# Optimization experiments

Measured on AMD Instinct MI355X. Metric: run time of the kernel, lower is better.

Reference implementation:

```python
import jax, jax.numpy as jnp
import numpy as np

D = 512  # feature_dim


def setup_inputs() -> dict:
    key = jax.random.key(0)
    ks = jax.random.split(key, 10)
    s = 1.0 / np.sqrt(D)
    s2 = 1.0 / np.sqrt(2 * D)
    return {
        "X": jax.random.normal(ks[0], (8, 2048, D), dtype=jnp.float32),
        "Y": jax.random.normal(ks[1], (8, 2048, D), dtype=jnp.float32),
        "W_xq": jax.random.uniform(ks[2], (D, D), jnp.float32, -s, s),
        "b_xq": jax.random.uniform(ks[3], (D,), jnp.float32, -s, s),
        "W_yq": jax.random.uniform(ks[4], (D, D), jnp.float32, -s, s),
        "b_yq": jax.random.uniform(ks[5], (D,), jnp.float32, -s, s),
        "W_fk": jax.random.uniform(ks[6], (D, 2 * D), jnp.float32, -s2, s2),
        "b_fk": jax.random.uniform(ks[7], (D,), jnp.float32, -s2, s2),
        "W_fv": jax.random.uniform(ks[8], (D, 2 * D), jnp.float32, -s2, s2),
        "b_fv": jax.random.uniform(ks[9], (D,), jnp.float32, -s2, s2),
    }


def reference(X, Y, W_xq, b_xq, W_yq, b_yq, W_fk, b_fk, W_fv, b_fv):
    # Dropout is evaluated in eval mode (identity).
    scale = 1.0 / jnp.sqrt(jnp.asarray(D, X.dtype))
    Q1 = jnp.einsum('bsd,ed->bse', X, W_xq) + b_xq  # [B,S,D]
    Q2 = jnp.einsum('bsd,ed->bse', Y, W_yq) + b_yq
    Q_cat = jnp.concatenate([Q1, Q2], axis=-1)      # [B,S,2D]
    K_f = jnp.einsum('bsc,ec->bse', Q_cat, W_fk) + b_fk
    V_f = jnp.einsum('bsc,ec->bse', Q_cat, W_fv) + b_fv

    def attend(Q):
        scores = jnp.einsum('bqd,bkd->bqk', Q, K_f) * scale  # [B,S,S]
        A = jax.nn.softmax(scores, axis=-1)
        return jnp.einsum('bqk,bkd->bqd', A, V_f)

    U_A1 = X + attend(Q1)
    U_A2 = Y + attend(Q2)
    return U_A1 + U_A2
```

## Files before the change

### kernel.cpp

```cpp
#include <hip/hip_runtime.h>


#define B_    8
#define S_    2048
#define D_    512
#define M_TOT (B_ * S_)

typedef __bf16 bf16_t;
typedef __bf16 bf16x8 __attribute__((ext_vector_type(8)));
typedef __bf16 bf16x4 __attribute__((ext_vector_type(4)));
typedef float  f32x4  __attribute__((ext_vector_type(4)));

typedef __attribute__((address_space(1))) const void* gas_cv;
typedef __attribute__((address_space(3))) void*       las_v;

__device__ __forceinline__ f32x4 mfma16(bf16x8 a, bf16x8 b, f32x4 c) {
    return __builtin_amdgcn_mfma_f32_16x16x32_bf16(a, b, c, 0, 0, 0);
}
__device__ __forceinline__ void load_lds16(const void* g, void* l) {
    __builtin_amdgcn_global_load_lds((gas_cv)g, (las_v)l, 16, 0, 0);
}

__global__ __launch_bounds__(256) void k_cvt(
    const float* __restrict__ X, const float* __restrict__ Y,
    const float* __restrict__ Wxq, const float* __restrict__ Wyq,
    const float* __restrict__ Wfk, const float* __restrict__ Wfv,
    bf16_t* __restrict__ Xb, bf16_t* __restrict__ Yb,
    bf16_t* __restrict__ Wb)
{
    const int tid = blockIdx.x * 256 + threadIdx.x;
    const int n4 = M_TOT * 512 / 4;
    for (int i = tid; i < n4; i += 2048 * 256) {
        const float4 x = *(const float4*)(X + (size_t)i * 4);
        bf16x4 px = { (bf16_t)x.x, (bf16_t)x.y, (bf16_t)x.z, (bf16_t)x.w };
        *(bf16x4*)(Xb + (size_t)i * 4) = px;
        const float4 y = *(const float4*)(Y + (size_t)i * 4);
        bf16x4 py = { (bf16_t)y.x, (bf16_t)y.y, (bf16_t)y.z, (bf16_t)y.w };
        *(bf16x4*)(Yb + (size_t)i * 4) = py;
    }
    if (tid < 393216) {
        const float* src; int sj;
        if (tid < 65536)       { src = Wxq; sj = tid; }
        else if (tid < 131072) { src = Wyq; sj = tid - 65536; }
        else if (tid < 262144) { src = Wfk; sj = tid - 131072; }
        else                   { src = Wfv; sj = tid - 262144; }
        const float4 v = *(const float4*)(src + (size_t)sj * 4);
        bf16x4 p = { (bf16_t)v.x, (bf16_t)v.y, (bf16_t)v.z, (bf16_t)v.w };
        *(bf16x4*)(Wb + (size_t)tid * 4) = p;
    }
}

__global__ __launch_bounds__(256) void k_qgemm_bb(
    const bf16_t* __restrict__ Xb, const bf16_t* __restrict__ Yb,
    const bf16_t* __restrict__ Wb,
    const float* __restrict__ bxq, const float* __restrict__ byq,
    bf16_t* __restrict__ Qcat)
{
    __shared__ __attribute__((aligned(16))) bf16_t Al[128 * 32];
    __shared__ __attribute__((aligned(16))) bf16_t Bl[128 * 32];
    const int m0 = blockIdx.y * 128;
    const int n0 = blockIdx.x * 128;
    const bool second = (n0 >= 512);
    const bf16_t* A   = second ? Yb : Xb;
    const bf16_t* W   = Wb + (second ? 262144 : 0);
    const float* bias = second ? byq : bxq;
    const int nw = n0 & 511;
    const int t    = threadIdx.x;
    const int lane = t & 63;
    const int wv   = t >> 6;
    const int wm   = (wv & 1) * 64;
    const int wn   = (wv >> 1) * 64;
    const int l15  = lane & 15;
    const int quad = lane >> 4;

    const int ar0 = t >> 2,          ac0 = (t & 3) * 8;
    const int ar1 = (256 + t) >> 2,  ac1 = ((256 + t) & 3) * 8;

    f32x4 acc[4][4] = {};

    for (int k0 = 0; k0 < 512; k0 += 32) {
        __syncthreads();
        load_lds16(A + (size_t)(m0 + ar0) * 512 + k0 + ac0, Al + t * 8);
        load_lds16(A + (size_t)(m0 + ar1) * 512 + k0 + ac1, Al + (256 + t) * 8);
        load_lds16(W + (size_t)(nw + ar0) * 512 + k0 + ac0, Bl + t * 8);
        load_lds16(W + (size_t)(nw + ar1) * 512 + k0 + ac1, Bl + (256 + t) * 8);
        __syncthreads();
        bf16x8 af[4], bfr[4];
#pragma unroll
        for (int i = 0; i < 4; ++i)
            af[i] = *(const bf16x8*)(Al + (wm + i * 16 + l15) * 32 + quad * 8);
#pragma unroll
        for (int i = 0; i < 4; ++i)
            bfr[i] = *(const bf16x8*)(Bl + (wn + i * 16 + l15) * 32 + quad * 8);
#pragma unroll
        for (int mt = 0; mt < 4; ++mt)
#pragma unroll
            for (int nt = 0; nt < 4; ++nt)
                acc[mt][nt] = mfma16(af[mt], bfr[nt], acc[mt][nt]);
    }

#pragma unroll
    for (int nt = 0; nt < 4; ++nt) {
        const int col  = n0 + wn + nt * 16 + l15;
        const float bv = bias[col & 511];
#pragma unroll
        for (int mt = 0; mt < 4; ++mt) {
            const int rowb = m0 + wm + mt * 16 + quad * 4;
#pragma unroll
            for (int r = 0; r < 4; ++r)
                Qcat[(size_t)(rowb + r) * 1024 + col] = (bf16_t)(acc[mt][nt][r] + bv);
        }
    }
}

__global__ __launch_bounds__(256) void k_kvgemm_bb(
    const bf16_t* __restrict__ Qcat,
    const bf16_t* __restrict__ Wfkb, const float* __restrict__ bfk,
    const bf16_t* __restrict__ Wfvb, const float* __restrict__ bfv,
    bf16_t* __restrict__ Kf, bf16_t* __restrict__ Vt)
{
    __shared__ __attribute__((aligned(16))) union {
        struct { bf16_t Al[128 * 32]; bf16_t Bl[128 * 32]; } g;
        bf16_t T[128 * 132];
    } sm;
    const int m0 = blockIdx.y * 128;
    const int n0 = blockIdx.x * 128;
    const bool isV = (n0 >= 512);
    const bf16_t* W   = isV ? Wfvb : Wfkb;
    const float* bias = isV ? bfv : bfk;
    const int nw = n0 & 511;
    const int t    = threadIdx.x;
    const int lane = t & 63;
    const int wv   = t >> 6;
    const int wm   = (wv & 1) * 64;
    const int wn   = (wv >> 1) * 64;
    const int l15  = lane & 15;
    const int quad = lane >> 4;

    const int ar0 = t >> 2,          ac0 = (t & 3) * 8;
    const int ar1 = (256 + t) >> 2,  ac1 = ((256 + t) & 3) * 8;

    f32x4 acc[4][4] = {};

    for (int k0 = 0; k0 < 1024; k0 += 32) {
        __syncthreads();
        load_lds16(Qcat + (size_t)(m0 + ar0) * 1024 + k0 + ac0, sm.g.Al + t * 8);
        load_lds16(Qcat + (size_t)(m0 + ar1) * 1024 + k0 + ac1, sm.g.Al + (256 + t) * 8);
        load_lds16(W + (size_t)(nw + ar0) * 1024 + k0 + ac0, sm.g.Bl + t * 8);
        load_lds16(W + (size_t)(nw + ar1) * 1024 + k0 + ac1, sm.g.Bl + (256 + t) * 8);
        __syncthreads();
        bf16x8 af[4], bfr[4];
#pragma unroll
        for (int i = 0; i < 4; ++i)
            af[i] = *(const bf16x8*)(sm.g.Al + (wm + i * 16 + l15) * 32 + quad * 8);
#pragma unroll
        for (int i = 0; i < 4; ++i)
            bfr[i] = *(const bf16x8*)(sm.g.Bl + (wn + i * 16 + l15) * 32 + quad * 8);
#pragma unroll
        for (int mt = 0; mt < 4; ++mt)
#pragma unroll
            for (int nt = 0; nt < 4; ++nt)
                acc[mt][nt] = mfma16(af[mt], bfr[nt], acc[mt][nt]);
    }

    if (!isV) {
#pragma unroll
        for (int nt = 0; nt < 4; ++nt) {
            const int col  = n0 + wn + nt * 16 + l15;
            const float bv = bias[col];
#pragma unroll
            for (int mt = 0; mt < 4; ++mt) {
                const int rowb = m0 + wm + mt * 16 + quad * 4;
#pragma unroll
                for (int r = 0; r < 4; ++r)
                    Kf[(size_t)(rowb + r) * 512 + col] = (bf16_t)(acc[mt][nt][r] + bv);
            }
        }
    } else {
        __syncthreads();
#pragma unroll
        for (int nt = 0; nt < 4; ++nt) {
            const int dl = wn + nt * 16 + l15;
            const float bv = bias[nw + dl];
#pragma unroll
            for (int mt = 0; mt < 4; ++mt) {
                const int sl = wm + mt * 16 + quad * 4;
#pragma unroll
                for (int r = 0; r < 4; ++r)
                    sm.T[dl * 132 + sl + r] = (bf16_t)(acc[mt][nt][r] + bv);
            }
        }
        __syncthreads();
        const int bb = m0 >> 11;
        const int sb = m0 & 2047;
        const int half = lane >> 5;
        const int sl4  = (lane & 31) * 4;
#pragma unroll
        for (int i = 0; i < 16; ++i) {
            const int dl = wv * 32 + i * 2 + half;
            const bf16x4 v = *(const bf16x4*)(sm.T + dl * 132 + sl4);
            *(bf16x4*)(Vt + (size_t)(bb * 512 + nw + dl) * 2048 + sb + sl4) = v;
        }
    }
}

__global__ __launch_bounds__(256) void k_qgemm(
    const float* __restrict__ X, const float* __restrict__ Y,
    const float* __restrict__ Wxq, const float* __restrict__ bxq,
    const float* __restrict__ Wyq, const float* __restrict__ byq,
    bf16_t* __restrict__ Qcat)
{
    __shared__ __attribute__((aligned(16))) bf16_t Al[128 * 40];
    __shared__ __attribute__((aligned(16))) bf16_t Bl[128 * 40];
    const int m0 = blockIdx.x * 128;
    const int n0 = blockIdx.y * 128;
    const bool second = (n0 >= 512);
    const float* A    = second ? Y : X;
    const float* W    = second ? Wyq : Wxq;
    const float* bias = second ? byq : bxq;
    const int nw = n0 & 511;
    const int t    = threadIdx.x;
    const int lane = t & 63;
    const int wv   = t >> 6;
    const int wm   = (wv & 1) * 64;
    const int wn   = (wv >> 1) * 64;
    const int l15  = lane & 15;
    const int quad = lane >> 4;

    f32x4 acc[4][4] = {};

    for (int k0 = 0; k0 < 512; k0 += 32) {
        __syncthreads();
#pragma unroll
        for (int p = 0; p < 4; ++p) {
            const int lin = p * 256 + t;
            const int row = lin >> 3;
            const int ch  = (lin & 7) * 4;
            const float4 va = *(const float4*)(A + (size_t)(m0 + row) * 512 + k0 + ch);
            bf16x4 pa = { (bf16_t)va.x, (bf16_t)va.y, (bf16_t)va.z, (bf16_t)va.w };
            *(bf16x4*)(Al + row * 40 + ch) = pa;
            const float4 vb = *(const float4*)(W + (size_t)(nw + row) * 512 + k0 + ch);
            bf16x4 pb = { (bf16_t)vb.x, (bf16_t)vb.y, (bf16_t)vb.z, (bf16_t)vb.w };
            *(bf16x4*)(Bl + row * 40 + ch) = pb;
        }
        __syncthreads();
        bf16x8 af[4], bfr[4];
#pragma unroll
        for (int i = 0; i < 4; ++i)
            af[i] = *(const bf16x8*)(Al + (wm + i * 16 + l15) * 40 + quad * 8);
#pragma unroll
        for (int i = 0; i < 4; ++i)
            bfr[i] = *(const bf16x8*)(Bl + (wn + i * 16 + l15) * 40 + quad * 8);
#pragma unroll
        for (int mt = 0; mt < 4; ++mt)
#pragma unroll
            for (int nt = 0; nt < 4; ++nt)
                acc[mt][nt] = mfma16(af[mt], bfr[nt], acc[mt][nt]);
    }

#pragma unroll
    for (int nt = 0; nt < 4; ++nt) {
        const int col  = n0 + wn + nt * 16 + l15;
        const float bv = bias[col & 511];
#pragma unroll
        for (int mt = 0; mt < 4; ++mt) {
            const int rowb = m0 + wm + mt * 16 + quad * 4;
#pragma unroll
            for (int r = 0; r < 4; ++r)
                Qcat[(size_t)(rowb + r) * 1024 + col] = (bf16_t)(acc[mt][nt][r] + bv);
        }
    }
}

__global__ __launch_bounds__(256) void k_kvgemm(
    const bf16_t* __restrict__ Qcat,
    const float* __restrict__ Wfk, const float* __restrict__ bfk,
    const float* __restrict__ Wfv, const float* __restrict__ bfv,
    bf16_t* __restrict__ Kf, bf16_t* __restrict__ Vt)
{
    __shared__ __attribute__((aligned(16))) union {
        struct { bf16_t Al[128 * 32]; bf16_t Bl[128 * 32]; } g;
        bf16_t T[128 * 132];
    } sm;
    const int m0 = blockIdx.x * 128;
    const int n0 = blockIdx.y * 128;
    const bool isV = (n0 >= 512);
    const float* W    = isV ? Wfv : Wfk;
    const float* bias = isV ? bfv : bfk;
    const int nw = n0 & 511;
    const int t    = threadIdx.x;
    const int lane = t & 63;
    const int wv   = t >> 6;
    const int wm   = (wv & 1) * 64;
    const int wn   = (wv >> 1) * 64;
    const int l15  = lane & 15;
    const int quad = lane >> 4;

    const int ar0 = t >> 2,          ac0 = (t & 3) * 8;
    const int ar1 = (256 + t) >> 2,  ac1 = ((256 + t) & 3) * 8;

    f32x4 acc[4][4] = {};

    for (int k0 = 0; k0 < 1024; k0 += 32) {
        __syncthreads();
        load_lds16(Qcat + (size_t)(m0 + ar0) * 1024 + k0 + ac0, sm.g.Al + t * 8);
        load_lds16(Qcat + (size_t)(m0 + ar1) * 1024 + k0 + ac1, sm.g.Al + (256 + t) * 8);
#pragma unroll
        for (int p = 0; p < 4; ++p) {
            const int lin = p * 256 + t;
            const int row = lin >> 3;
            const int ch  = (lin & 7) * 4;
            const float4 vb = *(const float4*)(W + (size_t)(nw + row) * 1024 + k0 + ch);
            bf16x4 pb = { (bf16_t)vb.x, (bf16_t)vb.y, (bf16_t)vb.z, (bf16_t)vb.w };
            *(bf16x4*)(sm.g.Bl + row * 32 + ch) = pb;
        }
        __syncthreads();
        bf16x8 af[4], bfr[4];
#pragma unroll
        for (int i = 0; i < 4; ++i)
            af[i] = *(const bf16x8*)(sm.g.Al + (wm + i * 16 + l15) * 32 + quad * 8);
#pragma unroll
        for (int i = 0; i < 4; ++i)
            bfr[i] = *(const bf16x8*)(sm.g.Bl + (wn + i * 16 + l15) * 32 + quad * 8);
#pragma unroll
        for (int mt = 0; mt < 4; ++mt)
#pragma unroll
            for (int nt = 0; nt < 4; ++nt)
                acc[mt][nt] = mfma16(af[mt], bfr[nt], acc[mt][nt]);
    }

    if (!isV) {
#pragma unroll
        for (int nt = 0; nt < 4; ++nt) {
            const int col  = n0 + wn + nt * 16 + l15;
            const float bv = bias[col];
#pragma unroll
            for (int mt = 0; mt < 4; ++mt) {
                const int rowb = m0 + wm + mt * 16 + quad * 4;
#pragma unroll
                for (int r = 0; r < 4; ++r)
                    Kf[(size_t)(rowb + r) * 512 + col] = (bf16_t)(acc[mt][nt][r] + bv);
            }
        }
    } else {
        __syncthreads();
#pragma unroll
        for (int nt = 0; nt < 4; ++nt) {
            const int dl = wn + nt * 16 + l15;
            const float bv = bias[nw + dl];
#pragma unroll
            for (int mt = 0; mt < 4; ++mt) {
                const int sl = wm + mt * 16 + quad * 4;
#pragma unroll
                for (int r = 0; r < 4; ++r)
                    sm.T[dl * 132 + sl + r] = (bf16_t)(acc[mt][nt][r] + bv);
            }
        }
        __syncthreads();
        const int bb = m0 >> 11;
        const int sb = m0 & 2047;
        const int half = lane >> 5;
        const int sl4  = (lane & 31) * 4;
#pragma unroll
        for (int i = 0; i < 16; ++i) {
            const int dl = wv * 32 + i * 2 + half;
            const bf16x4 v = *(const bf16x4*)(sm.T + dl * 132 + sl4);
            *(bf16x4*)(Vt + (size_t)(bb * 512 + nw + dl) * 2048 + sb + sl4) = v;
        }
    }
}

__global__ __launch_bounds__(256, 2) void k_attn(
    const bf16_t* __restrict__ Qcat, const bf16_t* __restrict__ Kf,
    const bf16_t* __restrict__ Vt,
    const float* __restrict__ X, const float* __restrict__ Y,
    float* __restrict__ out, bf16_t* __restrict__ attn,
    const int mode, const int which)
{
    __shared__ __attribute__((aligned(16))) bf16_t Kl[2][32 * 520];
    __shared__ __attribute__((aligned(16))) bf16_t Pl[2][64 * 40];
    __shared__ float lsumL[64];

    const int b = blockIdx.y;
    const int w = (mode == 0) ? (int)blockIdx.z : which;
    const int t    = threadIdx.x;
    const int lane = t & 63;
    const int wv   = t >> 6;
    const int l15  = lane & 15;
    const int quad = lane >> 4;
    const int q0   = blockIdx.x * 64;
    const int qw   = q0 + wv * 16;

    const bf16_t* Kbase = Kf + (size_t)b * S_ * 512;
    const bf16_t* Vbase = Vt + ((size_t)b * 512 + wv * 128) * S_;

    bf16x8 aq[16];
    {
        const bf16_t* qp = Qcat + (size_t)(b * S_ + qw + l15) * 1024 + w * 512 + quad * 8;
#pragma unroll
        for (int ks = 0; ks < 16; ++ks) aq[ks] = *(const bf16x8*)(qp + ks * 32);
    }

    f32x4 acc[4][8] = {};
    float lacc[4] = { 0.f, 0.f, 0.f, 0.f };
    const float sc2 = 0.04419417382415922f * 1.4426950408889634f;

#pragma unroll
    for (int p = 0; p < 8; ++p) {
        const int row = wv * 8 + p;
        load_lds16(Kbase + (size_t)row * 512 + lane * 8, Kl[0] + row * 520);
    }
    __syncthreads();

    {
#pragma unroll
        for (int p = 0; p < 8; ++p) {
            const int row = wv * 8 + p;
            load_lds16(Kbase + (size_t)(32 + row) * 512 + lane * 8, Kl[1] + row * 520);
        }
        f32x4 s0a = {}, s0b = {}, s1a = {}, s1b = {};
#pragma unroll
        for (int ks = 0; ks < 16; ks += 2) {
            const bf16x8 b0 = *(const bf16x8*)(Kl[0] + l15 * 520 + ks * 32 + quad * 8);
            const bf16x8 b1 = *(const bf16x8*)(Kl[0] + (16 + l15) * 520 + ks * 32 + quad * 8);
            const bf16x8 c0 = *(const bf16x8*)(Kl[0] + l15 * 520 + (ks + 1) * 32 + quad * 8);
            const bf16x8 c1 = *(const bf16x8*)(Kl[0] + (16 + l15) * 520 + (ks + 1) * 32 + quad * 8);
            s0a = mfma16(aq[ks], b0, s0a);
            s1a = mfma16(aq[ks], b1, s1a);
            s0b = mfma16(aq[ks + 1], c0, s0b);
            s1b = mfma16(aq[ks + 1], c1, s1b);
        }
        const f32x4 sA = s0a + s0b, sB = s1a + s1b;
#pragma unroll
        for (int r = 0; r < 4; ++r) {
            const float p0 = exp2f(sA[r] * sc2);
            const float p1 = exp2f(sB[r] * sc2);
            lacc[r] += p0 + p1;
            Pl[0][(wv * 16 + quad * 4 + r) * 40 + l15] = (bf16_t)p0;
            Pl[0][(wv * 16 + quad * 4 + r) * 40 + 16 + l15] = (bf16_t)p1;
        }
        __syncthreads();
    }

    for (int kb = 1; kb < 64; ++kb) {
        const int cur = kb & 1;
        const int prv = cur ^ 1;

        bf16x8 vb[8];
#pragma unroll
        for (int i = 0; i < 8; ++i)
            vb[i] = *(const bf16x8*)(Vbase + (size_t)(i * 16 + l15) * S_ +
                                     (kb - 1) * 32 + quad * 8);

        {
            const bf16_t* src = Kbase + (size_t)(kb + 1) * 32 * 512;
#pragma unroll
            for (int p = 0; p < 8; ++p) {
                const int row = wv * 8 + p;
                load_lds16(src + (size_t)row * 512 + lane * 8, Kl[prv] + row * 520);
            }
        }

        f32x4 s0a = {}, s0b = {}, s1a = {}, s1b = {};
#pragma unroll
        for (int ks = 0; ks < 16; ks += 2) {
            const bf16x8 b0 = *(const bf16x8*)(Kl[cur] + l15 * 520 + ks * 32 + quad * 8);
            const bf16x8 b1 = *(const bf16x8*)(Kl[cur] + (16 + l15) * 520 + ks * 32 + quad * 8);
            const bf16x8 c0 = *(const bf16x8*)(Kl[cur] + l15 * 520 + (ks + 1) * 32 + quad * 8);
            const bf16x8 c1 = *(const bf16x8*)(Kl[cur] + (16 + l15) * 520 + (ks + 1) * 32 + quad * 8);
            s0a = mfma16(aq[ks], b0, s0a);
            s1a = mfma16(aq[ks], b1, s1a);
            s0b = mfma16(aq[ks + 1], c0, s0b);
            s1b = mfma16(aq[ks + 1], c1, s1b);
        }

        {
            bf16x8 ap[4];
#pragma unroll
            for (int qt = 0; qt < 4; ++qt)
                ap[qt] = *(const bf16x8*)(Pl[prv] + (qt * 16 + l15) * 40 + quad * 8);
#pragma unroll
            for (int dt = 0; dt < 8; ++dt)
#pragma unroll
                for (int qt = 0; qt < 4; ++qt)
                    acc[qt][dt] = mfma16(ap[qt], vb[dt], acc[qt][dt]);
        }

        const f32x4 sA = s0a + s0b, sB = s1a + s1b;
#pragma unroll
        for (int r = 0; r < 4; ++r) {
            const float p0 = exp2f(sA[r] * sc2);
            const float p1 = exp2f(sB[r] * sc2);
            lacc[r] += p0 + p1;
            Pl[cur][(wv * 16 + quad * 4 + r) * 40 + l15] = (bf16_t)p0;
            Pl[cur][(wv * 16 + quad * 4 + r) * 40 + 16 + l15] = (bf16_t)p1;
        }

        __syncthreads();
    }

    {
        bf16x8 vb[8];
#pragma unroll
        for (int i = 0; i < 8; ++i)
            vb[i] = *(const bf16x8*)(Vbase + (size_t)(i * 16 + l15) * S_ +
                                     63 * 32 + quad * 8);
        bf16x8 ap[4];
#pragma unroll
        for (int qt = 0; qt < 4; ++qt)
            ap[qt] = *(const bf16x8*)(Pl[1] + (qt * 16 + l15) * 40 + quad * 8);
#pragma unroll
        for (int dt = 0; dt < 8; ++dt)
#pragma unroll
            for (int qt = 0; qt < 4; ++qt)
                acc[qt][dt] = mfma16(ap[qt], vb[dt], acc[qt][dt]);
    }

    {
        float lrow[4];
#pragma unroll
        for (int r = 0; r < 4; ++r) {
            float v = lacc[r];
#pragma unroll
            for (int off = 1; off < 16; off <<= 1) v += __shfl_xor(v, off, 64);
            lrow[r] = v;
        }
        if (l15 == 0) {
#pragma unroll
            for (int r = 0; r < 4; ++r) lsumL[wv * 16 + quad * 4 + r] = lrow[r];
        }
    }
    __syncthreads();

#pragma unroll
    for (int qt = 0; qt < 4; ++qt) {
        f32x4 inv;
#pragma unroll
        for (int r = 0; r < 4; ++r) inv[r] = 1.0f / lsumL[qt * 16 + quad * 4 + r];
#pragma unroll
        for (int dt = 0; dt < 8; ++dt) {
            const int d = wv * 128 + dt * 16 + l15;
#pragma unroll
            for (int r = 0; r < 4; ++r) {
                const float v = acc[qt][dt][r] * inv[r];
                const size_t idx =
                    (size_t)(b * S_ + q0 + qt * 16 + quad * 4 + r) * 512 + d;
                if (mode == 0)      attn[(size_t)w * M_TOT * 512 + idx] = (bf16_t)v;
                else if (mode == 1) out[idx] = X[idx] + Y[idx] + v;
                else                out[idx] += v;
            }
        }
    }
}

__global__ __launch_bounds__(256) void k_add(
    const float* __restrict__ X, const float* __restrict__ Y,
    const bf16_t* __restrict__ a0, const bf16_t* __restrict__ a1,
    float* __restrict__ out)
{
    const size_t i = ((size_t)blockIdx.x * 256 + threadIdx.x) * 4;
    const float4 x = *(const float4*)(X + i);
    const float4 y = *(const float4*)(Y + i);
    const bf16x4 v0 = *(const bf16x4*)(a0 + i);
    const bf16x4 v1 = *(const bf16x4*)(a1 + i);
    float4 o;
    o.x = x.x + y.x + (float)v0[0] + (float)v1[0];
    o.y = x.y + y.y + (float)v0[1] + (float)v1[1];
    o.z = x.z + y.z + (float)v0[2] + (float)v1[2];
    o.w = x.w + y.w + (float)v0[3] + (float)v1[3];
    *(float4*)(out + i) = o;
}

extern "C" void kernel_launch(void* const* d_in, const int* in_sizes, int n_in,
                              void* d_out, int out_size, void* d_ws, size_t ws_size,
                              hipStream_t stream)
{
    const float* X   = (const float*)d_in[0];
    const float* Y   = (const float*)d_in[1];
    const float* Wxq = (const float*)d_in[2];
    const float* bxq = (const float*)d_in[3];
    const float* Wyq = (const float*)d_in[4];
    const float* byq = (const float*)d_in[5];
    const float* Wfk = (const float*)d_in[6];
    const float* bfk = (const float*)d_in[7];
    const float* Wfv = (const float*)d_in[8];
    const float* bfv = (const float*)d_in[9];
    float* out = (float*)d_out;
    char*  ws  = (char*)d_ws;

    bf16_t* Qcat = (bf16_t*)(ws);
    bf16_t* Kf   = (bf16_t*)(ws + (size_t)33554432);
    bf16_t* Vt   = (bf16_t*)(ws + (size_t)50331648);
    bf16_t* Wb   = (bf16_t*)(ws + (size_t)67108864);
    bf16_t* attn = (bf16_t*)(ws + (size_t)67108864);
    bf16_t* Xb   = (bf16_t*)(ws + (size_t)83886080);
    bf16_t* Yb   = Kf;
    const bool big = ws_size >= (size_t)100663296;

    if (big) {
        k_cvt<<<dim3(2048), 256, 0, stream>>>(X, Y, Wxq, Wyq, Wfk, Wfv, Xb, Yb, Wb);
        k_qgemm_bb<<<dim3(8, 128), 256, 0, stream>>>(Xb, Yb, Wb, bxq, byq, Qcat);
        k_kvgemm_bb<<<dim3(8, 128), 256, 0, stream>>>(Qcat, Wb + 524288, bfk,
                                                      Wb + 1048576, bfv, Kf, Vt);
        k_attn<<<dim3(32, 8, 2), 256, 0, stream>>>(Qcat, Kf, Vt, X, Y, out, attn, 0, 0);
        k_add<<<dim3(8192), 256, 0, stream>>>(X, Y, attn, attn + (size_t)M_TOT * 512, out);
    } else {
        k_qgemm<<<dim3(128, 8), 256, 0, stream>>>(X, Y, Wxq, bxq, Wyq, byq, Qcat);
        k_kvgemm<<<dim3(128, 8), 256, 0, stream>>>(Qcat, Wfk, bfk, Wfv, bfv, Kf, Vt);
        k_attn<<<dim3(32, 8, 1), 256, 0, stream>>>(Qcat, Kf, Vt, X, Y, out, attn, 1, 0);
        k_attn<<<dim3(32, 8, 1), 256, 0, stream>>>(Qcat, Kf, Vt, X, Y, out, attn, 2, 1);
    }
}
```

Before: 438.5 us.

## Fuse both attention heads into one 512-thread block sharing K tiles

Adds a new attention kernel in which each 512-thread block processes both query sets (Q1 and Q2) for the same 64-row query tile, so each K tile staged in LDS is reused by two groups of four waves. It replaces the launch with grid z=2, where each query set separately reloaded K and V from global memory. The cost is a larger block with more LDS for the doubled P buffers, and V fragments are still read per wave straight from global memory. Softmax is computed without max subtraction, relying on bounded scores.

```diff
diff --git a/kernel.cpp b/kernel.cpp
--- a/kernel.cpp
+++ b/kernel.cpp
@@ -370,6 +370,185 @@
     }
 }
 
+__global__ __launch_bounds__(512, 2) void k_attn2(
+    const bf16_t* __restrict__ Qcat, const bf16_t* __restrict__ Kf,
+    const bf16_t* __restrict__ Vt, bf16_t* __restrict__ attn)
+{
+    __shared__ __attribute__((aligned(16))) bf16_t Kl[2][32 * 520];
+    __shared__ __attribute__((aligned(16))) bf16_t Pl[2][2][64 * 40];
+    __shared__ float lsumL[2][64];
+
+    const int b = blockIdx.y;
+    const int t    = threadIdx.x;
+    const int lane = t & 63;
+    const int wv   = t >> 6;
+    const int hd   = wv >> 2;
+    const int wq   = wv & 3;
+    const int l15  = lane & 15;
+    const int quad = lane >> 4;
+    const int q0   = blockIdx.x * 64;
+    const int qw   = q0 + wq * 16;
+
+    const bf16_t* Kbase = Kf + (size_t)b * S_ * 512;
+    const bf16_t* Vbase = Vt + ((size_t)b * 512 + wq * 128) * S_;
+
+    bf16x8 aq[16];
+    {
+        const bf16_t* qp = Qcat + (size_t)(b * S_ + qw + l15) * 1024 + hd * 512 + quad * 8;
+#pragma unroll
+        for (int ks = 0; ks < 16; ++ks) aq[ks] = *(const bf16x8*)(qp + ks * 32);
+    }
+
+    f32x4 acc[4][8] = {};
+    float lacc[4] = { 0.f, 0.f, 0.f, 0.f };
+    const float sc2 = 0.04419417382415922f * 1.4426950408889634f;
+
+#pragma unroll
+    for (int p = 0; p < 4; ++p) {
+        const int row = wv * 4 + p;
+        load_lds16(Kbase + (size_t)row * 512 + lane * 8, Kl[0] + row * 520);
+    }
+    __syncthreads();
+
+    {
+#pragma unroll
+        for (int p = 0; p < 4; ++p) {
+            const int row = wv * 4 + p;
+            load_lds16(Kbase + (size_t)(32 + row) * 512 + lane * 8, Kl[1] + row * 520);
+        }
+        f32x4 s0a = {}, s0b = {}, s1a = {}, s1b = {};
+#pragma unroll
+        for (int ks = 0; ks < 16; ks += 2) {
+            const bf16x8 b0 = *(const bf16x8*)(Kl[0] + l15 * 520 + ks * 32 + quad * 8);
+            const bf16x8 b1 = *(const bf16x8*)(Kl[0] + (16 + l15) * 520 + ks * 32 + quad * 8);
+            const bf16x8 c0 = *(const bf16x8*)(Kl[0] + l15 * 520 + (ks + 1) * 32 + quad * 8);
+            const bf16x8 c1 = *(const bf16x8*)(Kl[0] + (16 + l15) * 520 + (ks + 1) * 32 + quad * 8);
+            s0a = mfma16(aq[ks], b0, s0a);
+            s1a = mfma16(aq[ks], b1, s1a);
+            s0b = mfma16(aq[ks + 1], c0, s0b);
+            s1b = mfma16(aq[ks + 1], c1, s1b);
+        }
+        const f32x4 sA = s0a + s0b, sB = s1a + s1b;
+#pragma unroll
+        for (int r = 0; r < 4; ++r) {
+            const float p0 = exp2f(sA[r] * sc2);
+            const float p1 = exp2f(sB[r] * sc2);
+            lacc[r] += p0 + p1;
+            Pl[hd][0][(wq * 16 + quad * 4 + r) * 40 + l15] = (bf16_t)p0;
+            Pl[hd][0][(wq * 16 + quad * 4 + r) * 40 + 16 + l15] = (bf16_t)p1;
+        }
+        __syncthreads();
+    }
+
+    for (int kb = 1; kb < 64; ++kb) {
+        const int cur = kb & 1;
+        const int prv = cur ^ 1;
+
+        bf16x8 vb[8];
+#pragma unroll
+        for (int i = 0; i < 8; ++i)
+            vb[i] = *(const bf16x8*)(Vbase + (size_t)(i * 16 + l15) * S_ +
+                                     (kb - 1) * 32 + quad * 8);
+
+        {
+            const bf16_t* src = Kbase + (size_t)(kb + 1) * 32 * 512;
+#pragma unroll
+            for (int p = 0; p < 4; ++p) {
+                const int row = wv * 4 + p;
+                load_lds16(src + (size_t)row * 512 + lane * 8, Kl[prv] + row * 520);
+            }
+        }
+
+        f32x4 s0a = {}, s0b = {}, s1a = {}, s1b = {};
+#pragma unroll
+        for (int ks = 0; ks < 16; ks += 2) {
+            const bf16x8 b0 = *(const bf16x8*)(Kl[cur] + l15 * 520 + ks * 32 + quad * 8);
+            const bf16x8 b1 = *(const bf16x8*)(Kl[cur] + (16 + l15) * 520 + ks * 32 + quad * 8);
+            const bf16x8 c0 = *(const bf16x8*)(Kl[cur] + l15 * 520 + (ks + 1) * 32 + quad * 8);
+            const bf16x8 c1 = *(const bf16x8*)(Kl[cur] + (16 + l15) * 520 + (ks + 1) * 32 + quad * 8);
+            s0a = mfma16(aq[ks], b0, s0a);
+            s1a = mfma16(aq[ks], b1, s1a);
+            s0b = mfma16(aq[ks + 1], c0, s0b);
+            s1b = mfma16(aq[ks + 1], c1, s1b);
+        }
+
+        {
+            bf16x8 ap[4];
+#pragma unroll
+            for (int qt = 0; qt < 4; ++qt)
+                ap[qt] = *(const bf16x8*)(Pl[hd][prv] + (qt * 16 + l15) * 40 + quad * 8);
+#pragma unroll
+            for (int dt = 0; dt < 8; ++dt)
+#pragma unroll
+                for (int qt = 0; qt < 4; ++qt)
+                    acc[qt][dt] = mfma16(ap[qt], vb[dt], acc[qt][dt]);
+        }
+
+        const f32x4 sA = s0a + s0b, sB = s1a + s1b;
+#pragma unroll
+        for (int r = 0; r < 4; ++r) {
+            const float p0 = exp2f(sA[r] * sc2);
+            const float p1 = exp2f(sB[r] * sc2);
+            lacc[r] += p0 + p1;
+            Pl[hd][cur][(wq * 16 + quad * 4 + r) * 40 + l15] = (bf16_t)p0;
+            Pl[hd][cur][(wq * 16 + quad * 4 + r) * 40 + 16 + l15] = (bf16_t)p1;
+        }
+
+        __syncthreads();
+    }
+
+    {
+        bf16x8 vb[8];
+#pragma unroll
+        for (int i = 0; i < 8; ++i)
+            vb[i] = *(const bf16x8*)(Vbase + (size_t)(i * 16 + l15) * S_ +
+                                     63 * 32 + quad * 8);
+        bf16x8 ap[4];
+#pragma unroll
+        for (int qt = 0; qt < 4; ++qt)
+            ap[qt] = *(const bf16x8*)(Pl[hd][1] + (qt * 16 + l15) * 40 + quad * 8);
+#pragma unroll
+        for (int dt = 0; dt < 8; ++dt)
+#pragma unroll
+            for (int qt = 0; qt < 4; ++qt)
+                acc[qt][dt] = mfma16(ap[qt], vb[dt], acc[qt][dt]);
+    }
+
+    {
+        float lrow[4];
+#pragma unroll
+        for (int r = 0; r < 4; ++r) {
+            float v = lacc[r];
+#pragma unroll
+            for (int off = 1; off < 16; off <<= 1) v += __shfl_xor(v, off, 64);
+            lrow[r] = v;
+        }
+        if (l15 == 0) {
+#pragma unroll
+            for (int r = 0; r < 4; ++r) lsumL[hd][wq * 16 + quad * 4 + r] = lrow[r];
+        }
+    }
+    __syncthreads();
+
+#pragma unroll
+    for (int qt = 0; qt < 4; ++qt) {
+        f32x4 inv;
+#pragma unroll
+        for (int r = 0; r < 4; ++r) inv[r] = 1.0f / lsumL[hd][qt * 16 + quad * 4 + r];
+#pragma unroll
+        for (int dt = 0; dt < 8; ++dt) {
+            const int d = wq * 128 + dt * 16 + l15;
+#pragma unroll
+            for (int r = 0; r < 4; ++r) {
+                const float v = acc[qt][dt][r] * inv[r];
+                const size_t idx =
+                    (size_t)(b * S_ + q0 + qt * 16 + quad * 4 + r) * 512 + d;
+                attn[(size_t)hd * M_TOT * 512 + idx] = (bf16_t)v;
+            }
+        }
+    }
+}
+
 __global__ __launch_bounds__(256, 2) void k_attn(
     const bf16_t* __restrict__ Qcat, const bf16_t* __restrict__ Kf,
     const bf16_t* __restrict__ Vt,
@@ -602,7 +781,7 @@
         k_qgemm_bb<<<dim3(8, 128), 256, 0, stream>>>(Xb, Yb, Wb, bxq, byq, Qcat);
         k_kvgemm_bb<<<dim3(8, 128), 256, 0, stream>>>(Qcat, Wb + 524288, bfk,
                                                       Wb + 1048576, bfv, Kf, Vt);
-        k_attn<<<dim3(32, 8, 2), 256, 0, stream>>>(Qcat, Kf, Vt, X, Y, out, attn, 0, 0);
+        k_attn2<<<dim3(32, 8), 512, 0, stream>>>(Qcat, Kf, Vt, attn);
         k_add<<<dim3(8192), 256, 0, stream>>>(X, Y, attn, attn + (size_t)M_TOT * 512, out);
     } else {
         k_qgemm<<<dim3(128, 8), 256, 0, stream>>>(X, Y, Wxq, bxq, Wyq, byq, Qcat);
```

Measured after the change: 458.1 us. +4.5%, slower.
